# Optimization experiments

Hardware: AMD Instinct MI355X
Metric: run time of the kernel (lower is better)

The kernel has to match this reference:

```python
import jax, jax.numpy as jnp
import numpy as np

DIM = 1024
NUM_HEADS = 16
HEAD_DIM = DIM // NUM_HEADS
SCALE = HEAD_DIM ** -0.5


def setup_inputs() -> dict:
    key = jax.random.key(0)
    k_x, k_qkv, k_pw, k_pb = jax.random.split(key, 4)
    B, L = 2, 2048
    x = jax.random.normal(k_x, (B, L, DIM), dtype=jnp.float32)
    # nn.Linear weights are [out, in]; stored the same way here.
    w_qkv = jax.random.normal(k_qkv, (3 * DIM, DIM), dtype=jnp.float32) * (DIM ** -0.5)
    w_proj = jax.random.normal(k_pw, (DIM, DIM), dtype=jnp.float32) * (DIM ** -0.5)
    b_proj = jax.random.normal(k_pb, (DIM,), dtype=jnp.float32) * 0.01
    return {"x": x, "w_qkv": w_qkv, "w_proj": w_proj, "b_proj": b_proj}


def reference(x, w_qkv, w_proj, b_proj):
    B, L, P = x.shape
    H, D = NUM_HEADS, HEAD_DIM
    # qkv projection (no bias): [B, L, 3*P]
    qkv = jnp.einsum('blp,op->blo', x, w_qkv)
    qkv = qkv.reshape(B, L, 3, H, D).transpose(2, 0, 3, 1, 4)  # [3, B, H, L, D]
    q, k, v = qkv[0], qkv[1], qkv[2]
    attn = jnp.einsum('bhld,bhmd->bhlm', q, k) * SCALE  # [B, H, L, L]
    attn = jax.nn.softmax(attn, axis=-1)
    out = jnp.einsum('bhlm,bhmd->bhld', attn, v)  # [B, H, L, D]
    out = out.transpose(0, 2, 1, 3).reshape(B, L, P)
    out = jnp.einsum('blp,op->blo', out, w_proj) + b_proj
    return out
```

## Files before the change

### kernel.cpp

```cpp
#include <hip/hip_runtime.h>
#include <hip/hip_bf16.h>
#include <stdint.h>
#include <stddef.h>

typedef short s16x8 __attribute__((ext_vector_type(8)));
typedef float f32x4  __attribute__((ext_vector_type(4)));
typedef float f32x16 __attribute__((ext_vector_type(16)));
typedef unsigned int u32x2 __attribute__((ext_vector_type(2)));

#define MFMA16(a, b, c) __builtin_amdgcn_mfma_f32_16x16x32_bf16((a), (b), (c), 0, 0, 0)
#define MFMA32(a, b, c) __builtin_amdgcn_mfma_f32_32x32x16_bf16((a), (b), (c), 0, 0, 0)
#define EXP2(x) __builtin_amdgcn_exp2f(x)

__device__ __forceinline__ unsigned short f2bf(float f) {
  union { float f; uint32_t u; } v; v.f = f;
  uint32_t u = v.u;
  return (unsigned short)((u + 0x7FFFu + ((u >> 16) & 1u)) >> 16);
}

__device__ __forceinline__ unsigned int pack_bf16x2(float a, float b) {
  __hip_bfloat162 h = __float22bfloat162_rn(make_float2(a, b));
  union { __hip_bfloat162 h; unsigned int u; } c; c.h = h;
  return c.u;
}

__device__ __forceinline__ void load_lds16(const void* gsrc, void* ldst) {
  void* gp = const_cast<void*>(gsrc);
  __builtin_amdgcn_global_load_lds(
      (__attribute__((address_space(1))) void*)gp,
      (__attribute__((address_space(3))) void*)ldst, 16, 0, 0);
}

#define B_    2
#define L_    2048
#define DIM_  1024
#define NH_   16
#define HD_   64
#define MTOT  (B_ * L_)
#define QSCALE_ 0.18033688011112042f
#define SMSHIFT_ 16.0f

__global__ void cvt_all(const float* __restrict__ x, const float* __restrict__ wq,
                        const float* __restrict__ wp,
                        unsigned short* __restrict__ xb, unsigned short* __restrict__ wqb,
                        unsigned short* __restrict__ wpb) {
  const int X4 = 1048576, Q4 = 786432;
  int i = blockIdx.x * 256 + threadIdx.x;
  const float* in; unsigned short* out; int idx;
  if (i < X4)            { in = x;  out = xb;  idx = i; }
  else if (i < X4 + Q4)  { in = wq; out = wqb; idx = i - X4; }
  else                   { in = wp; out = wpb; idx = i - X4 - Q4; }
  float4 v = ((const float4*)in)[idx];
  uint2 r;
  r.x = pack_bf16x2(v.x, v.y);
  r.y = pack_bf16x2(v.z, v.w);
  ((uint2*)out)[idx] = r;
}

__global__ void __launch_bounds__(512)
gemm_qkv(const unsigned short* __restrict__ A,
         const unsigned short* __restrict__ Bw,
         unsigned short* __restrict__ Qb,
         unsigned short* __restrict__ Kb,
         unsigned short* __restrict__ Vt) {
  const int K = DIM_;
  __shared__ __attribute__((aligned(16))) unsigned short Al[2][128 * 32];
  __shared__ __attribute__((aligned(16))) unsigned short Bl[2][128 * 32];
  const int tid  = threadIdx.x;
  const int lane = tid & 63, wv = tid >> 6;
  const int g = lane >> 4, lr = lane & 15;
  const int wr = wv >> 2, wc = wv & 3;
  const int m0 = blockIdx.x * 128, n0 = blockIdx.y * 128;

  f32x4 acc[4][2];
  const f32x4 zero = {0.f, 0.f, 0.f, 0.f};
#pragma unroll
  for (int i = 0; i < 4; i++) { acc[i][0] = zero; acc[i][1] = zero; }

#define STAGE_G(buf, k0)                                                              \
  {                                                                                   \
    int c   = tid;                                                                    \
    int row = c >> 2, kc = c & 3;                                                     \
    int ks  = (kc ^ ((row ^ (row >> 2)) & 3)) * 8;                                    \
    load_lds16(A  + (size_t)(m0 + row) * K + (k0) + ks, (char*)&Al[buf][0] + c * 16); \
    load_lds16(Bw + (size_t)(n0 + row) * K + (k0) + ks, (char*)&Bl[buf][0] + c * 16); \
  }

  STAGE_G(0, 0);
  __syncthreads();
  const int NTk = K >> 5;
  for (int t = 0; t < NTk; ++t) {
    const int cur = t & 1;
    if (t + 1 < NTk) STAGE_G(cur ^ 1, (t + 1) * 32);

    s16x8 af[4], bf[2];
#pragma unroll
    for (int mi = 0; mi < 4; mi++) {
      int row = wr * 64 + mi * 16 + lr;
      int ch  = g ^ ((row ^ (row >> 2)) & 3);
      af[mi]  = *(const s16x8*)((const char*)&Al[cur][0] + row * 64 + ch * 16);
    }
#pragma unroll
    for (int ni = 0; ni < 2; ni++) {
      int row = wc * 32 + ni * 16 + lr;
      int ch  = g ^ ((row ^ (row >> 2)) & 3);
      bf[ni]  = *(const s16x8*)((const char*)&Bl[cur][0] + row * 64 + ch * 16);
    }
    __builtin_amdgcn_s_setprio(1);
#pragma unroll
    for (int mi = 0; mi < 4; mi++)
#pragma unroll
      for (int ni = 0; ni < 2; ni++)
        acc[mi][ni] = MFMA16(af[mi], bf[ni], acc[mi][ni]);
    __builtin_amdgcn_s_setprio(0);
    __syncthreads();
  }
#undef STAGE_G

#pragma unroll
  for (int mi = 0; mi < 4; mi++)
#pragma unroll
    for (int ni = 0; ni < 2; ni++) {
      int ncol = n0 + wc * 32 + ni * 16 + lr;
      int s = ncol >> 10;
      int h = (ncol >> 6) & 15;
      int d = ncol & 63;
#pragma unroll
      for (int j = 0; j < 4; j++) {
        int m = m0 + wr * 64 + mi * 16 + g * 4 + j;
        int b = m >> 11, l = m & 2047;
        size_t bh = (size_t)(b * NH_ + h);
        if (s == 0)      Qb[(bh * L_ + l) * HD_ + d] = f2bf(acc[mi][ni][j] * QSCALE_);
        else if (s == 1) Kb[(bh * L_ + l) * HD_ + d] = f2bf(acc[mi][ni][j]);
        else             Vt[(bh * HD_ + d) * L_ + l] = f2bf(acc[mi][ni][j]);
      }
    }
}

__global__ void __launch_bounds__(512)
gemm_proj(const unsigned short* __restrict__ A,
          const unsigned short* __restrict__ Bw,
          float* __restrict__ Cout,
          const float* __restrict__ bias) {
  const int K = DIM_, N = DIM_;
  __shared__ __attribute__((aligned(16))) unsigned short Al[2][128 * 32];
  __shared__ __attribute__((aligned(16))) unsigned short Bl[2][64 * 32];
  const int tid  = threadIdx.x;
  const int lane = tid & 63, wv = tid >> 6;
  const int g = lane >> 4, lr = lane & 15;
  const int wr = wv >> 2, wc = wv & 3;
  const int m0 = blockIdx.x * 128, n0 = blockIdx.y * 64;

  f32x4 acc[4];
  const f32x4 zero = {0.f, 0.f, 0.f, 0.f};
#pragma unroll
  for (int i = 0; i < 4; i++) acc[i] = zero;

#define STAGE_P(buf, k0)                                                              \
  {                                                                                   \
    int c   = tid;                                                                    \
    int row = c >> 2, kc = c & 3;                                                     \
    int ks  = (kc ^ ((row ^ (row >> 2)) & 3)) * 8;                                    \
    load_lds16(A + (size_t)(m0 + row) * K + (k0) + ks, (char*)&Al[buf][0] + c * 16);  \
    if (tid < 256) {                                                                  \
      load_lds16(Bw + (size_t)(n0 + row) * K + (k0) + ks, (char*)&Bl[buf][0] + c * 16); \
    }                                                                                 \
  }

  STAGE_P(0, 0);
  __syncthreads();
  const int NTk = K >> 5;
  for (int t = 0; t < NTk; ++t) {
    const int cur = t & 1;
    if (t + 1 < NTk) STAGE_P(cur ^ 1, (t + 1) * 32);

    s16x8 af[4], bf;
#pragma unroll
    for (int mi = 0; mi < 4; mi++) {
      int row = wr * 64 + mi * 16 + lr;
      int ch  = g ^ ((row ^ (row >> 2)) & 3);
      af[mi]  = *(const s16x8*)((const char*)&Al[cur][0] + row * 64 + ch * 16);
    }
    {
      int row = wc * 16 + lr;
      int ch  = g ^ ((row ^ (row >> 2)) & 3);
      bf      = *(const s16x8*)((const char*)&Bl[cur][0] + row * 64 + ch * 16);
    }
    __builtin_amdgcn_s_setprio(1);
#pragma unroll
    for (int mi = 0; mi < 4; mi++)
      acc[mi] = MFMA16(af[mi], bf, acc[mi]);
    __builtin_amdgcn_s_setprio(0);
    __syncthreads();
  }
#undef STAGE_P

#pragma unroll
  for (int mi = 0; mi < 4; mi++) {
    int ncol = n0 + wc * 16 + lr;
    float bv = bias[ncol];
#pragma unroll
    for (int j = 0; j < 4; j++) {
      int m = m0 + wr * 64 + mi * 16 + g * 4 + j;
      Cout[(size_t)m * N + ncol] = acc[mi][j] + bv;
    }
  }
}

__global__ void __launch_bounds__(512, 4)
attn_fwd(const unsigned short* __restrict__ Qb,
         const unsigned short* __restrict__ Kb,
         const unsigned short* __restrict__ Vt,
         unsigned short* __restrict__ Ob) {
  __shared__ __attribute__((aligned(16))) unsigned short Kl[2][2][64 * 64];
  __shared__ __attribute__((aligned(16))) unsigned short Vl[2][2][64 * 64];

  const int tid  = threadIdx.x;
  const int lane = tid & 63, w = tid >> 6;
  const int sp = w >> 2, wvl = w & 3;
  const int hi = lane >> 5, lq = lane & 31;
  const int f   = blockIdx.y * 16 + blockIdx.x;
  const int swz = (f & 7) * 64 + (f >> 3);
  const int qt = swz & 15, bh = swz >> 4;

  const unsigned short* Qh = Qb + (size_t)bh * L_ * HD_;
  const unsigned short* Kh = Kb + (size_t)bh * L_ * HD_;
  const unsigned short* Vh = Vt + (size_t)bh * HD_ * L_;
  const int q0 = qt * 128 + wvl * 32;
  const int kvbase = sp * (L_ / 2);

  s16x8 qf[4];
#pragma unroll
  for (int ks = 0; ks < 4; ++ks)
    qf[ks] = *(const s16x8*)(Qh + (size_t)(q0 + lq) * HD_ + ks * 16 + hi * 8);

  f32x16 o0, o1;
#pragma unroll
  for (int r = 0; r < 16; ++r) { o0[r] = 0.f; o1[r] = 0.f; }
  float rsum = 0.f;

#define STAGE(buf, kv0)                                                          \
  {                                                                              \
    _Pragma("unroll")                                                            \
    for (int it = 0; it < 2; ++it) {                                             \
      int c = it * 256 + wvl * 64 + lane;                                        \
      int row = c >> 3, cc = c & 7;                                              \
      int cs = (cc ^ (row & 7)) * 8;                                             \
      load_lds16(Kh + (size_t)((kv0) + row) * HD_ + cs, (char*)&Kl[sp][buf][0] + c * 16); \
      load_lds16(Vh + (size_t)row * L_ + (kv0) + cs,    (char*)&Vl[sp][buf][0] + c * 16); \
    }                                                                            \
  }

  STAGE(0, kvbase);
  __syncthreads();

  const int NT = (L_ / 2) / 64;
  for (int t = 0; t < NT; ++t) {
    const int cur = t & 1;
    if (t + 1 < NT) STAGE(cur ^ 1, kvbase + (t + 1) * 64);

    const unsigned short* KL = &Kl[sp][cur][0];
    const unsigned short* VL = &Vl[sp][cur][0];

    f32x16 s0, s1;
#pragma unroll
    for (int r = 0; r < 16; ++r) { s0[r] = -SMSHIFT_; s1[r] = -SMSHIFT_; }
    __builtin_amdgcn_s_setprio(1);
#pragma unroll
    for (int ks = 0; ks < 4; ++ks) {
      int cc = ((ks << 1) | hi) ^ (lq & 7);
      s16x8 k0 = *(const s16x8*)((const char*)KL + lq * 128 + cc * 16);
      s0 = MFMA32(k0, qf[ks], s0);
      s16x8 k1 = *(const s16x8*)((const char*)KL + (32 + lq) * 128 + cc * 16);
      s1 = MFMA32(k1, qf[ks], s1);
    }
    __builtin_amdgcn_s_setprio(0);

#pragma unroll
    for (int r = 0; r < 16; ++r) { s0[r] = EXP2(s0[r]); s1[r] = EXP2(s1[r]); }

    {
      f32x16 ta;
#pragma unroll
      for (int r = 0; r < 16; ++r) ta[r] = s0[r] + s1[r];
#pragma unroll
      for (int wd = 8; wd >= 1; wd >>= 1)
#pragma unroll
        for (int r = 0; r < 8; ++r) if (r < wd) ta[r] += ta[r + wd];
      rsum += ta[0];
    }

#pragma unroll
    for (int st = 0; st < 2; ++st) {
      unsigned int pd[8];
#pragma unroll
      for (int r2 = 0; r2 < 8; ++r2)
        pd[r2] = st ? pack_bf16x2(s1[2 * r2], s1[2 * r2 + 1])
                    : pack_bf16x2(s0[2 * r2], s0[2 * r2 + 1]);
      __builtin_amdgcn_s_setprio(1);
#pragma unroll
      for (int ksl = 0; ksl < 2; ++ksl) {
        u32x2 e0 = __builtin_amdgcn_permlane32_swap(pd[4 * ksl + 0], pd[4 * ksl + 2], false, false);
        u32x2 e1 = __builtin_amdgcn_permlane32_swap(pd[4 * ksl + 1], pd[4 * ksl + 3], false, false);
        union { unsigned int u[4]; s16x8 v; } pa;
        pa.u[0] = e0[0];
        pa.u[1] = e1[0];
        pa.u[2] = e0[1];
        pa.u[3] = e1[1];
#pragma unroll
        for (int dt = 0; dt < 2; ++dt) {
          int row = dt * 32 + lq;
          int cc = (4 * st + 2 * ksl + hi) ^ (row & 7);
          s16x8 vf = *(const s16x8*)((const char*)VL + row * 128 + cc * 16);
          if (dt == 0) o0 = MFMA32(vf, pa.v, o0);
          else         o1 = MFMA32(vf, pa.v, o1);
        }
      }
      __builtin_amdgcn_s_setprio(0);
    }

    __syncthreads();
  }
#undef STAGE

  {
    union { float f; unsigned u; } ru; ru.f = rsum;
    u32x2 rs = __builtin_amdgcn_permlane32_swap(ru.u, ru.u, false, false);
    union { unsigned u; float f; } r0, r1; r0.u = rs[0]; r1.u = rs[1];
    rsum = r0.f + r1.f;
  }

  float* Osh = (float*)&Kl[0][0][0];
  float* Lsh = (float*)&Vl[0][0][0];
  if (sp == 1) {
#pragma unroll
    for (int r = 0; r < 16; ++r) {
      int d = (r & 3) + 8 * (r >> 2) + 4 * hi;
      Osh[wvl * 2048 + d * 32 + lq]        = o0[r];
      Osh[wvl * 2048 + (d + 32) * 32 + lq] = o1[r];
    }
    if (hi == 0) Lsh[wvl * 32 + lq] = rsum;
  }
  __syncthreads();
  if (sp == 0) {
    const float inv = 1.0f / (rsum + Lsh[wvl * 32 + lq]);
#pragma unroll
    for (int r = 0; r < 16; ++r) {
      int d = (r & 3) + 8 * (r >> 2) + 4 * hi;
      o0[r] = (o0[r] + Osh[wvl * 2048 + d * 32 + lq]) * inv;
      o1[r] = (o1[r] + Osh[wvl * 2048 + (d + 32) * 32 + lq]) * inv;
    }
    const int b = bh >> 4, h = bh & 15;
    const int q = q0 + lq;
    size_t base = ((size_t)(b * L_ + q)) * DIM_ + h * HD_;
#pragma unroll
    for (int dt = 0; dt < 2; ++dt)
#pragma unroll
      for (int r2 = 0; r2 < 8; ++r2) {
        int d = dt * 32 + 8 * (r2 >> 1) + 4 * hi + 2 * (r2 & 1);
        float a = dt ? o1[2 * r2] : o0[2 * r2];
        float c = dt ? o1[2 * r2 + 1] : o0[2 * r2 + 1];
        unsigned int pv = pack_bf16x2(a, c);
        *(unsigned int*)((unsigned short*)Ob + base + d) = pv;
      }
  }
}

extern "C" void kernel_launch(void* const* d_in, const int* in_sizes, int n_in,
                              void* d_out, int out_size, void* d_ws, size_t ws_size,
                              hipStream_t stream) {
  const float* x      = (const float*)d_in[0];
  const float* w_qkv  = (const float*)d_in[1];
  const float* w_proj = (const float*)d_in[2];
  const float* b_proj = (const float*)d_in[3];
  float* out = (float*)d_out;

  const size_t N_X    = (size_t)MTOT * DIM_;
  const size_t N_WQKV = (size_t)3 * DIM_ * DIM_;
  const size_t N_WPRJ = (size_t)DIM_ * DIM_;
  const size_t N_QKV  = (size_t)B_ * NH_ * L_ * HD_;

  unsigned short* xb     = (unsigned short*)d_ws;
  unsigned short* wqkvb  = xb + N_X;
  unsigned short* wprojb = wqkvb + N_WQKV;
  unsigned short* Qb     = wprojb + N_WPRJ;
  unsigned short* Kb     = Qb + N_QKV;
  unsigned short* Vt     = Kb + N_QKV;
  unsigned short* Obuf   = Vt + N_QKV;

  cvt_all<<<8192, 256, 0, stream>>>(x, w_qkv, w_proj, xb, wqkvb, wprojb);

  dim3 g1(MTOT / 128, (3 * DIM_) / 128);
  gemm_qkv<<<g1, 512, 0, stream>>>(xb, wqkvb, Qb, Kb, Vt);

  dim3 g2(L_ / 128, B_ * NH_);
  attn_fwd<<<g2, 512, 0, stream>>>(Qb, Kb, Vt, Obuf);

  dim3 g3(MTOT / 128, DIM_ / 64);
  gemm_proj<<<g3, 512, 0, stream>>>(Obuf, wprojb, out, b_proj);
}
```

Before: 117.9 us.

## Retile QKV GEMM to 256x256 blocks with quarter-staged LDS pipeline

The QKV projection GEMM moves from 128x128 tiles with BK=32 to 256x256 tiles with BK=64. The next K-tile is prefetched in four quarter chunks interleaved with four MFMA phases, guarded by explicit vmcnt waits and barriers. This raises arithmetic intensity per block and cuts global and LDS traffic per FLOP. In exchange, the grid shrinks to 192 blocks, fewer than the CU count, and register and LDS pressure rise (128KB LDS).

```diff
diff --git a/kernel.cpp b/kernel.cpp
--- a/kernel.cpp
+++ b/kernel.cpp
@@ -11,6 +11,7 @@
 #define MFMA16(a, b, c) __builtin_amdgcn_mfma_f32_16x16x32_bf16((a), (b), (c), 0, 0, 0)
 #define MFMA32(a, b, c) __builtin_amdgcn_mfma_f32_32x32x16_bf16((a), (b), (c), 0, 0, 0)
 #define EXP2(x) __builtin_amdgcn_exp2f(x)
+#define WAITCNT_VM(N) asm volatile("s_waitcnt vmcnt(" #N ")" ::: "memory")
 
 __device__ __forceinline__ unsigned short f2bf(float f) {
   union { float f; uint32_t u; } v; v.f = f;
@@ -64,70 +65,137 @@
          unsigned short* __restrict__ Kb,
          unsigned short* __restrict__ Vt) {
   const int K = DIM_;
-  __shared__ __attribute__((aligned(16))) unsigned short Al[2][128 * 32];
-  __shared__ __attribute__((aligned(16))) unsigned short Bl[2][128 * 32];
+  const int NTK = 16;
+  __shared__ __attribute__((aligned(16))) char smem[2][4][16384];
+
   const int tid  = threadIdx.x;
   const int lane = tid & 63, wv = tid >> 6;
   const int g = lane >> 4, lr = lane & 15;
   const int wr = wv >> 2, wc = wv & 3;
-  const int m0 = blockIdx.x * 128, n0 = blockIdx.y * 128;
-
-  f32x4 acc[4][2];
+  const int m0 = blockIdx.x * 256, n0 = blockIdx.y * 256;
+
+  f32x4 acc[8][4];
   const f32x4 zero = {0.f, 0.f, 0.f, 0.f};
 #pragma unroll
-  for (int i = 0; i < 4; i++) { acc[i][0] = zero; acc[i][1] = zero; }
-
-#define STAGE_G(buf, k0)                                                              \
-  {                                                                                   \
-    int c   = tid;                                                                    \
-    int row = c >> 2, kc = c & 3;                                                     \
-    int ks  = (kc ^ ((row ^ (row >> 2)) & 3)) * 8;                                    \
-    load_lds16(A  + (size_t)(m0 + row) * K + (k0) + ks, (char*)&Al[buf][0] + c * 16); \
-    load_lds16(Bw + (size_t)(n0 + row) * K + (k0) + ks, (char*)&Bl[buf][0] + c * 16); \
-  }
-
-  STAGE_G(0, 0);
-  __syncthreads();
-  const int NTk = K >> 5;
-  for (int t = 0; t < NTk; ++t) {
-    const int cur = t & 1;
-    if (t + 1 < NTk) STAGE_G(cur ^ 1, (t + 1) * 32);
-
-    s16x8 af[4], bf[2];
-#pragma unroll
-    for (int mi = 0; mi < 4; mi++) {
-      int row = wr * 64 + mi * 16 + lr;
-      int ch  = g ^ ((row ^ (row >> 2)) & 3);
-      af[mi]  = *(const s16x8*)((const char*)&Al[cur][0] + row * 64 + ch * 16);
-    }
-#pragma unroll
-    for (int ni = 0; ni < 2; ni++) {
-      int row = wc * 32 + ni * 16 + lr;
-      int ch  = g ^ ((row ^ (row >> 2)) & 3);
-      bf[ni]  = *(const s16x8*)((const char*)&Bl[cur][0] + row * 64 + ch * 16);
-    }
-    __builtin_amdgcn_s_setprio(1);
-#pragma unroll
-    for (int mi = 0; mi < 4; mi++)
-#pragma unroll
-      for (int ni = 0; ni < 2; ni++)
-        acc[mi][ni] = MFMA16(af[mi], bf[ni], acc[mi][ni]);
-    __builtin_amdgcn_s_setprio(0);
-    __syncthreads();
-  }
-#undef STAGE_G
-
-#pragma unroll
-  for (int mi = 0; mi < 4; mi++)
-#pragma unroll
-    for (int ni = 0; ni < 2; ni++) {
-      int ncol = n0 + wc * 32 + ni * 16 + lr;
+  for (int i = 0; i < 8; i++)
+#pragma unroll
+    for (int j = 0; j < 4; j++) acc[i][j] = zero;
+
+#define STAGE_HT(buf, ht, kt)                                                      \
+  {                                                                                \
+    const unsigned short* base_ = ((ht) < 2)                                       \
+        ? (A  + (size_t)(m0 + (ht) * 128) * K)                                     \
+        : (Bw + (size_t)(n0 + ((ht) - 2) * 128) * K);                              \
+    _Pragma("unroll")                                                              \
+    for (int pass = 0; pass < 2; ++pass) {                                         \
+      int c = pass * 512 + tid;                                                    \
+      int row = c >> 3, slot = c & 7;                                              \
+      load_lds16(base_ + (size_t)row * K + (kt) * 64 + ((slot ^ (row & 7)) * 8),   \
+                 &smem[buf][ht][c * 16]);                                          \
+    }                                                                              \
+  }
+
+#define FRAG(region, r, q16)                                                       \
+  (*(const s16x8*)&(region)[(r) * 128 + (((q16) ^ ((r) & 7)) * 16)])
+
+  STAGE_HT(0, 0, 0); STAGE_HT(0, 1, 0); STAGE_HT(0, 2, 0); STAGE_HT(0, 3, 0);
+
+  s16x8 af[4][2], bf[4][2];
+
+  for (int kt = 0; kt < NTK; ++kt) {
+    const int b = kt & 1;
+    const char* Ah = &smem[b][wr][0];
+    const char* Bh = &smem[b][2 + (wc >> 1)][0];
+    const int rb = (wc & 1) * 64;
+    const bool have = (kt + 1 < NTK);
+
+    if (have) { STAGE_HT(b ^ 1, 0, kt + 1); WAITCNT_VM(2); }
+    else      { WAITCNT_VM(0); }
+    __syncthreads();
+#pragma unroll
+    for (int mi = 0; mi < 4; ++mi)
+#pragma unroll
+      for (int ks = 0; ks < 2; ++ks)
+        af[mi][ks] = FRAG(Ah, mi * 16 + lr, ks * 4 + g);
+#pragma unroll
+    for (int ni = 0; ni < 2; ++ni)
+#pragma unroll
+      for (int ks = 0; ks < 2; ++ks)
+        bf[ni][ks] = FRAG(Bh, rb + ni * 16 + lr, ks * 4 + g);
+    __builtin_amdgcn_s_setprio(1);
+#pragma unroll
+    for (int mi = 0; mi < 4; ++mi)
+#pragma unroll
+      for (int ni = 0; ni < 2; ++ni)
+#pragma unroll
+        for (int ks = 0; ks < 2; ++ks)
+          acc[mi][ni] = MFMA16(af[mi][ks], bf[ni][ks], acc[mi][ni]);
+    __builtin_amdgcn_s_setprio(0);
+    __syncthreads();
+
+#pragma unroll
+    for (int ni = 2; ni < 4; ++ni)
+#pragma unroll
+      for (int ks = 0; ks < 2; ++ks)
+        bf[ni][ks] = FRAG(Bh, rb + ni * 16 + lr, ks * 4 + g);
+    if (have) STAGE_HT(b ^ 1, 1, kt + 1);
+    __syncthreads();
+    __builtin_amdgcn_s_setprio(1);
+#pragma unroll
+    for (int mi = 0; mi < 4; ++mi)
+#pragma unroll
+      for (int ni = 2; ni < 4; ++ni)
+#pragma unroll
+        for (int ks = 0; ks < 2; ++ks)
+          acc[mi][ni] = MFMA16(af[mi][ks], bf[ni][ks], acc[mi][ni]);
+    __builtin_amdgcn_s_setprio(0);
+    __syncthreads();
+
+#pragma unroll
+    for (int mi = 0; mi < 4; ++mi)
+#pragma unroll
+      for (int ks = 0; ks < 2; ++ks)
+        af[mi][ks] = FRAG(Ah, 64 + mi * 16 + lr, ks * 4 + g);
+    if (have) STAGE_HT(b ^ 1, 2, kt + 1);
+    __syncthreads();
+    __builtin_amdgcn_s_setprio(1);
+#pragma unroll
+    for (int mi = 0; mi < 4; ++mi)
+#pragma unroll
+      for (int ni = 0; ni < 2; ++ni)
+#pragma unroll
+        for (int ks = 0; ks < 2; ++ks)
+          acc[4 + mi][ni] = MFMA16(af[mi][ks], bf[ni][ks], acc[4 + mi][ni]);
+    __builtin_amdgcn_s_setprio(0);
+    __syncthreads();
+
+    if (have) STAGE_HT(b ^ 1, 3, kt + 1);
+    __syncthreads();
+    __builtin_amdgcn_s_setprio(1);
+#pragma unroll
+    for (int mi = 0; mi < 4; ++mi)
+#pragma unroll
+      for (int ni = 2; ni < 4; ++ni)
+#pragma unroll
+        for (int ks = 0; ks < 2; ++ks)
+          acc[4 + mi][ni] = MFMA16(af[mi][ks], bf[ni][ks], acc[4 + mi][ni]);
+    __builtin_amdgcn_s_setprio(0);
+    __syncthreads();
+  }
+#undef STAGE_HT
+#undef FRAG
+
+#pragma unroll
+  for (int mi = 0; mi < 8; ++mi)
+#pragma unroll
+    for (int ni = 0; ni < 4; ++ni) {
+      int ncol = n0 + wc * 64 + ni * 16 + lr;
       int s = ncol >> 10;
       int h = (ncol >> 6) & 15;
       int d = ncol & 63;
 #pragma unroll
       for (int j = 0; j < 4; j++) {
-        int m = m0 + wr * 64 + mi * 16 + g * 4 + j;
+        int m = m0 + wr * 128 + mi * 16 + g * 4 + j;
         int b = m >> 11, l = m & 2047;
         size_t bh = (size_t)(b * NH_ + h);
         if (s == 0)      Qb[(bh * L_ + l) * HD_ + d] = f2bf(acc[mi][ni][j] * QSCALE_);
@@ -390,7 +458,7 @@
 
   cvt_all<<<8192, 256, 0, stream>>>(x, w_qkv, w_proj, xb, wqkvb, wprojb);
 
-  dim3 g1(MTOT / 128, (3 * DIM_) / 128);
+  dim3 g1(MTOT / 256, (3 * DIM_) / 256);
   gemm_qkv<<<g1, 512, 0, stream>>>(xb, wqkvb, Qb, Kb, Vt);
 
   dim3 g2(L_ / 128, B_ * NH_);
```

Result: slower. 154.6 us (+31.2%).
